# Kernel optimization log

Hardware: AMD Instinct MI355X
Metric: run time of the kernel (lower is better)

Reference implementation:

```python
import jax, jax.numpy as jnp
import numpy as np

EPS = 1e-3  # keras LayerNormalization default epsilon


def layer_norm(x, gamma, beta):
    mean = jnp.mean(x, axis=-1, keepdims=True)
    var = jnp.var(x, axis=-1, keepdims=True)
    return (x - mean) * jax.lax.rsqrt(var + EPS) * gamma + beta


def setup_inputs() -> dict:
    key = jax.random.key(0)
    ks = jax.random.split(key, 8)
    B, H, W, C = 16, 64, 64, 512
    IC = C // 8  # intermediate_channel = 64
    x = jax.random.normal(ks[0], (B, H, W, C), dtype=jnp.float32)
    s = 1.0 / np.sqrt(C)
    w_f = jax.random.normal(ks[1], (C, IC), dtype=jnp.float32) * s
    w_h = jax.random.normal(ks[2], (C, IC), dtype=jnp.float32) * s
    w_fgh = jax.random.normal(ks[3], (IC, C), dtype=jnp.float32) / np.sqrt(IC)
    gamma_f = jnp.ones((IC,), jnp.float32)
    beta_f = jnp.zeros((IC,), jnp.float32)
    gamma_h = jnp.ones((IC,), jnp.float32)
    beta_h = jnp.zeros((IC,), jnp.float32)
    gamma_fgh = jnp.ones((C,), jnp.float32)
    beta_fgh = jnp.zeros((C,), jnp.float32)
    scale = jnp.ones((1,), jnp.float32)  # non-negative scalar gate
    return {"x": x, "w_f": w_f, "w_h": w_h, "w_fgh": w_fgh,
            "gamma_f": gamma_f, "beta_f": beta_f,
            "gamma_h": gamma_h, "beta_h": beta_h,
            "gamma_fgh": gamma_fgh, "beta_fgh": beta_fgh,
            "scale": scale}


def reference(x, w_f, w_h, w_fgh, gamma_f, beta_f, gamma_h, beta_h,
              gamma_fgh, beta_fgh, scale):
    # NOTE: faithful to the source, which (re)uses w_f/LN_f for BOTH f and g,
    # and combines f and g with an ELEMENTWISE multiply (not a matmul).
    g = layer_norm(jnp.einsum("bhwc,ci->bhwi", x, w_f), gamma_f, beta_f)  # (B,H,W,IC)
    f = jnp.transpose(g, (0, 2, 1, 3))  # Permute(2,1,3): (B,W,H,IC)
    h = layer_norm(jnp.einsum("bhwc,ci->bhwi", x, w_h), gamma_h, beta_h)
    a = jax.nn.softmax(f * g, axis=1)  # softmax over axis 1 (H==W required)
    y = jnp.einsum("bhwi,ic->bhwc", a * h, w_fgh)
    y = layer_norm(y, gamma_fgh, beta_fgh) * scale  # scalar gate
    return x + y  # residual add
```

## Files before the change

### kernel.cpp

```cpp
#include <hip/hip_runtime.h>

#define EPSN 1e-3f

typedef __attribute__((ext_vector_type(8))) short short8;
typedef __attribute__((ext_vector_type(4))) float floatx4;

__device__ __forceinline__ unsigned f2bf_pack(float a, float b) {
    unsigned ua = __builtin_bit_cast(unsigned, a);
    ua += 0x7FFF + ((ua >> 16) & 1);
    unsigned ub = __builtin_bit_cast(unsigned, b);
    ub += 0x7FFF + ((ub >> 16) & 1);
    return (ua >> 16) | (ub & 0xFFFF0000u);
}
__device__ __forceinline__ unsigned short f2bf(float f) {
    unsigned u = __builtin_bit_cast(unsigned, f);
    u += 0x7FFF + ((u >> 16) & 1);
    return (unsigned short)(u >> 16);
}
__device__ __forceinline__ float bf2f(unsigned short u) {
    unsigned v = ((unsigned)u) << 16;
    return __builtin_bit_cast(float, v);
}

__global__ void k0_convert(const float* __restrict__ w_f,
                           const float* __restrict__ w_h,
                           const float* __restrict__ w_fgh,
                           unsigned short* __restrict__ Wgh,
                           unsigned short* __restrict__ Wf3)
{
    int tid = blockIdx.x * 256 + threadIdx.x;
    if (tid < 8192) {
        int n16 = tid & 15, k8 = (tid >> 4) & 63, ntile = tid >> 10;
        int n = ntile * 16 + n16;
        const float* src = (n < 64) ? (w_f + n) : (w_h + (n - 64));
        unsigned short o[8];
        #pragma unroll
        for (int j = 0; j < 8; ++j) o[j] = f2bf(src[(size_t)(k8 * 8 + j) * 64]);
        *(uint4*)&Wgh[(size_t)tid * 8] = *(const uint4*)o;
    } else if (tid < 12288) {
        int id = tid - 8192;
        int n16 = id & 15, k8 = (id >> 4) & 7, ntile = id >> 7;
        int n = ntile * 16 + n16;
        unsigned short o[8];
        #pragma unroll
        for (int j = 0; j < 8; ++j) o[j] = f2bf(w_fgh[(size_t)(k8 * 8 + j) * 512 + n]);
        *(uint4*)&Wf3[(size_t)id * 8] = *(const uint4*)o;
    }
}

__global__ __launch_bounds__(256, 4) void k1_gemm_ln(
    const float* __restrict__ x,
    const unsigned short* __restrict__ Wgh,
    const float* __restrict__ gamma_f, const float* __restrict__ beta_f,
    const float* __restrict__ gamma_h, const float* __restrict__ beta_h,
    float* __restrict__ g_out, unsigned short* __restrict__ h_out)
{
    const int t = threadIdx.x;
    const int lane = t & 63;
    const int wv = t >> 6;
    const int quad = lane >> 4;
    const int n16 = lane & 15;
    const int row_base = blockIdx.x * 64 + wv * 16;

    floatx4 acc[8];
    #pragma unroll
    for (int ct = 0; ct < 8; ++ct) acc[ct] = (floatx4){0.f, 0.f, 0.f, 0.f};

    const float* xrow = x + (size_t)(row_base + n16) * 512 + quad * 8;

    float4 u = *(const float4*)(xrow);
    float4 v = *(const float4*)(xrow + 4);

    #pragma unroll
    for (int c = 0; c < 16; ++c) {
        float4 un = u, vn = v;
        if (c < 15) {
            un = *(const float4*)(xrow + (c + 1) * 32);
            vn = *(const float4*)(xrow + (c + 1) * 32 + 4);
        }
        union { short8 s; uint4 q; } cvt;
        cvt.q = make_uint4(f2bf_pack(u.x, u.y), f2bf_pack(u.z, u.w),
                           f2bf_pack(v.x, v.y), f2bf_pack(v.z, v.w));
        short8 a = cvt.s;
        #pragma unroll
        for (int ct = 0; ct < 8; ++ct) {
            short8 b = *(const short8*)&Wgh[(size_t)(((ct * 64) + c * 4 + quad) * 16 + n16) * 8];
            acc[ct] = __builtin_amdgcn_mfma_f32_16x16x32_bf16(a, b, acc[ct], 0, 0, 0);
        }
        u = un; v = vn;
    }

    #pragma unroll
    for (int half = 0; half < 2; ++half) {
        float s[4] = {0.f, 0.f, 0.f, 0.f}, s2[4] = {0.f, 0.f, 0.f, 0.f};
        #pragma unroll
        for (int c0 = 0; c0 < 4; ++c0) {
            int ct = half * 4 + c0;
            #pragma unroll
            for (int r = 0; r < 4; ++r) {
                float val = acc[ct][r];
                s[r] += val; s2[r] += val * val;
            }
        }
        #pragma unroll
        for (int off = 1; off <= 8; off <<= 1)
            #pragma unroll
            for (int r = 0; r < 4; ++r) {
                s[r]  += __shfl_xor(s[r],  off, 64);
                s2[r] += __shfl_xor(s2[r], off, 64);
            }
        float mean[4], rstd[4];
        #pragma unroll
        for (int r = 0; r < 4; ++r) {
            mean[r] = s[r] * (1.f / 64.f);
            float var = s2[r] * (1.f / 64.f) - mean[r] * mean[r];
            rstd[r] = rsqrtf(var + EPSN);
        }
        #pragma unroll
        for (int c0 = 0; c0 < 4; ++c0) {
            int ct = half * 4 + c0;
            int col = c0 * 16 + n16;
            float gm = half ? gamma_h[col] : gamma_f[col];
            float bt = half ? beta_h[col]  : beta_f[col];
            #pragma unroll
            for (int r = 0; r < 4; ++r) {
                int row = row_base + quad * 4 + r;
                float val = (acc[ct][r] - mean[r]) * rstd[r] * gm + bt;
                if (half == 0)
                    g_out[(size_t)row * 64 + col] = val;
                else
                    h_out[(size_t)row * 64 + col] = f2bf(val);
            }
        }
    }
}

__global__ __launch_bounds__(256, 4) void k2_softmax(
    const float* __restrict__ g_in,
    const unsigned short* __restrict__ h_in,
    unsigned short* __restrict__ t_out)
{
    __shared__ float S[64 * 64];
    __shared__ float Hm[64 * 64];
    __shared__ float pmax[4 * 64];
    __shared__ float psum[4 * 64];
    __shared__ float colmax[64];
    __shared__ float colinv[64];

    const int t = threadIdx.x;
    const int b = blockIdx.x >> 6;
    const int w = blockIdx.x & 63;
    const size_t base1 = (size_t)(b * 64 + w) * 4096;

    #pragma unroll
    for (int i = 0; i < 16; ++i) {
        int e = t + i * 256;
        int hh = e >> 6, ii = e & 63;
        size_t idx2 = ((size_t)((b * 64 + hh) * 64 + w)) * 64 + ii;
        S[e]  = g_in[base1 + e] * g_in[idx2];
        Hm[e] = bf2f(h_in[idx2]);
    }
    __syncthreads();

    const int q = t >> 6;
    const int i = t & 63;
    float m = -1e30f;
    #pragma unroll
    for (int r = 0; r < 16; ++r)
        m = fmaxf(m, S[(q * 16 + r) * 64 + i]);
    pmax[q * 64 + i] = m;
    __syncthreads();
    if (t < 64)
        colmax[i] = fmaxf(fmaxf(pmax[i], pmax[64 + i]),
                          fmaxf(pmax[128 + i], pmax[192 + i]));
    __syncthreads();
    const float cm = colmax[i];
    float s = 0.f;
    #pragma unroll
    for (int r = 0; r < 16; ++r) {
        int idx = (q * 16 + r) * 64 + i;
        float e = __expf(S[idx] - cm);
        S[idx] = e;
        s += e;
    }
    psum[q * 64 + i] = s;
    __syncthreads();
    if (t < 64)
        colinv[i] = 1.f / (psum[i] + psum[64 + i] + psum[128 + i] + psum[192 + i]);
    __syncthreads();
    const float ci = colinv[i];
    #pragma unroll
    for (int r = 0; r < 16; ++r) {
        int hh = q * 16 + r;
        int idx = hh * 64 + i;
        size_t row_g = (size_t)((b * 64 + hh) * 64 + w);
        t_out[row_g * 64 + i] = f2bf(S[idx] * ci * Hm[idx]);
    }
}

__global__ __launch_bounds__(256, 4) void k3_gemm_ln_res(
    const unsigned short* __restrict__ tmat,
    const unsigned short* __restrict__ Wf3,
    const float* __restrict__ gamma, const float* __restrict__ beta,
    const float* __restrict__ scale,
    const float* __restrict__ x,
    float* __restrict__ out)
{
    __shared__ float bounce[4][16 * 132];
    __shared__ float2 exch[4][16];

    const int t = threadIdx.x;
    const int lane = t & 63;
    const int wv = t >> 6;
    const int quad = lane >> 4;
    const int n16 = lane & 15;
    const int rowtile = blockIdx.x * 2 + (wv >> 1);
    const int half = wv & 1;

    const unsigned short* trow = tmat + (size_t)(rowtile * 16 + n16) * 64 + quad * 8;
    short8 a0 = *(const short8*)trow;
    short8 a1 = *(const short8*)(trow + 32);

    floatx4 acc[16];
    #pragma unroll
    for (int nt = 0; nt < 16; ++nt) acc[nt] = (floatx4){0.f, 0.f, 0.f, 0.f};
    #pragma unroll
    for (int nt = 0; nt < 16; ++nt) {
        int ngt = half * 16 + nt;
        short8 b0 = *(const short8*)&Wf3[(size_t)((ngt * 8 + quad) * 16 + n16) * 8];
        short8 b1 = *(const short8*)&Wf3[(size_t)((ngt * 8 + 4 + quad) * 16 + n16) * 8];
        acc[nt] = __builtin_amdgcn_mfma_f32_16x16x32_bf16(a0, b0, acc[nt], 0, 0, 0);
        acc[nt] = __builtin_amdgcn_mfma_f32_16x16x32_bf16(a1, b1, acc[nt], 0, 0, 0);
    }

    float s[4] = {0.f, 0.f, 0.f, 0.f}, s2[4] = {0.f, 0.f, 0.f, 0.f};
    #pragma unroll
    for (int nt = 0; nt < 16; ++nt)
        #pragma unroll
        for (int r = 0; r < 4; ++r) {
            float v = acc[nt][r];
            s[r] += v; s2[r] += v * v;
        }
    #pragma unroll
    for (int off = 1; off <= 8; off <<= 1)
        #pragma unroll
        for (int r = 0; r < 4; ++r) {
            s[r]  += __shfl_xor(s[r],  off, 64);
            s2[r] += __shfl_xor(s2[r], off, 64);
        }
    if (n16 == 0) {
        #pragma unroll
        for (int r = 0; r < 4; ++r)
            exch[wv][quad * 4 + r] = make_float2(s[r], s2[r]);
    }
    __syncthreads();
    float mean[4], rstd[4];
    #pragma unroll
    for (int r = 0; r < 4; ++r) {
        float2 o = exch[wv ^ 1][quad * 4 + r];
        float st = s[r] + o.x, st2 = s2[r] + o.y;
        mean[r] = st * (1.f / 512.f);
        float var = st2 * (1.f / 512.f) - mean[r] * mean[r];
        rstd[r] = rsqrtf(var + EPSN);
    }
    const float sc = scale[0];

    #pragma unroll
    for (int chunk = 0; chunk < 2; ++chunk) {
        __syncthreads();
        #pragma unroll
        for (int n0 = 0; n0 < 8; ++n0) {
            int nt = chunk * 8 + n0;
            int col = half * 256 + nt * 16 + n16;
            float gm = gamma[col], bt = beta[col];
            #pragma unroll
            for (int r = 0; r < 4; ++r)
                bounce[wv][(quad * 4 + r) * 132 + n0 * 16 + n16] =
                    sc * ((acc[nt][r] - mean[r]) * rstd[r] * gm + bt);
        }
        __syncthreads();
        #pragma unroll
        for (int pass = 0; pass < 8; ++pass) {
            int row = pass * 2 + (lane >> 5);
            int coff = (lane & 31) * 4;
            float4 v = *(const float4*)&bounce[wv][row * 132 + coff];
            size_t gidx = ((size_t)rowtile * 16 + row) * 512 + half * 256 + chunk * 128 + coff;
            float4 xv = *(const float4*)&x[gidx];
            float4 o;
            o.x = xv.x + v.x; o.y = xv.y + v.y; o.z = xv.z + v.z; o.w = xv.w + v.w;
            *(float4*)&out[gidx] = o;
        }
    }
}

extern "C" void kernel_launch(void* const* d_in, const int* in_sizes, int n_in,
                              void* d_out, int out_size, void* d_ws, size_t ws_size,
                              hipStream_t stream) {
    const float* x         = (const float*)d_in[0];
    const float* w_f       = (const float*)d_in[1];
    const float* w_h       = (const float*)d_in[2];
    const float* w_fgh     = (const float*)d_in[3];
    const float* gamma_f   = (const float*)d_in[4];
    const float* beta_f    = (const float*)d_in[5];
    const float* gamma_h   = (const float*)d_in[6];
    const float* beta_h    = (const float*)d_in[7];
    const float* gamma_fgh = (const float*)d_in[8];
    const float* beta_fgh  = (const float*)d_in[9];
    const float* scale     = (const float*)d_in[10];
    float* out = (float*)d_out;

    char* wsb = (char*)d_ws;
    float* g            = (float*)wsb;
    unsigned short* h   = (unsigned short*)(wsb + 16777216);
    unsigned short* tm  = (unsigned short*)(wsb + 25165824);
    unsigned short* Wgh = (unsigned short*)(wsb + 33554432);
    unsigned short* Wf3 = (unsigned short*)(wsb + 33685504);

    k0_convert<<<48, 256, 0, stream>>>(w_f, w_h, w_fgh, Wgh, Wf3);
    k1_gemm_ln<<<1024, 256, 0, stream>>>(x, Wgh, gamma_f, beta_f,
                                         gamma_h, beta_h, g, h);
    k2_softmax<<<1024, 256, 0, stream>>>(g, h, tm);
    k3_gemm_ln_res<<<2048, 256, 0, stream>>>(tm, Wf3, gamma_fgh, beta_fgh,
                                             scale, x, out);
}
```

Baseline: 310.6 us.

## Stage Wgh B-tiles through double-buffered LDS via global_load_lds in k1

```diff
diff --git a/kernel.cpp b/kernel.cpp
--- a/kernel.cpp
+++ b/kernel.cpp
@@ -20,6 +20,13 @@
 __device__ __forceinline__ float bf2f(unsigned short u) {
     unsigned v = ((unsigned)u) << 16;
     return __builtin_bit_cast(float, v);
+}
+
+__device__ __forceinline__ void gload_lds16(const unsigned short* g, unsigned short* l) {
+    __builtin_amdgcn_global_load_lds(
+        (const __attribute__((address_space(1))) unsigned int*)g,
+        (__attribute__((address_space(3))) unsigned int*)l,
+        16, 0, 0);
 }
 
 __global__ void k0_convert(const float* __restrict__ w_f,
@@ -55,6 +62,8 @@
     const float* __restrict__ gamma_h, const float* __restrict__ beta_h,
     float* __restrict__ g_out, unsigned short* __restrict__ h_out)
 {
+    __shared__ unsigned short Blds[2][8192];
+
     const int t = threadIdx.x;
     const int lane = t & 63;
     const int wv = t >> 6;
@@ -67,27 +76,53 @@
     for (int ct = 0; ct < 8; ++ct) acc[ct] = (floatx4){0.f, 0.f, 0.f, 0.f};
 
     const float* xrow = x + (size_t)(row_base + n16) * 512 + quad * 8;
-
-    float4 u = *(const float4*)(xrow);
-    float4 v = *(const float4*)(xrow + 4);
-
-    #pragma unroll
-    for (int c = 0; c < 16; ++c) {
-        float4 un = u, vn = v;
-        if (c < 15) {
-            un = *(const float4*)(xrow + (c + 1) * 32);
-            vn = *(const float4*)(xrow + (c + 1) * 32 + 4);
-        }
-        union { short8 s; uint4 q; } cvt;
-        cvt.q = make_uint4(f2bf_pack(u.x, u.y), f2bf_pack(u.z, u.w),
-                           f2bf_pack(v.x, v.y), f2bf_pack(v.z, v.w));
-        short8 a = cvt.s;
-        #pragma unroll
-        for (int ct = 0; ct < 8; ++ct) {
-            short8 b = *(const short8*)&Wgh[(size_t)(((ct * 64) + c * 4 + quad) * 16 + n16) * 8];
-            acc[ct] = __builtin_amdgcn_mfma_f32_16x16x32_bf16(a, b, acc[ct], 0, 0, 0);
-        }
-        u = un; v = vn;
+    const unsigned short* bsrc = Wgh + (size_t)lane * 8;
+
+    auto stage = [&](int par, int ch) {
+        #pragma unroll
+        for (int i = 0; i < 4; ++i) {
+            int s = wv * 4 + i;
+            int cl = s >> 3, ct = s & 7;
+            gload_lds16(bsrc + (size_t)ct * 8192 + (ch * 2 + cl) * 512,
+                        &Blds[par][s * 512]);
+        }
+    };
+
+    stage(0, 0);
+    float4 u[2], v[2];
+    u[0] = *(const float4*)(xrow);
+    v[0] = *(const float4*)(xrow + 4);
+    u[1] = *(const float4*)(xrow + 32);
+    v[1] = *(const float4*)(xrow + 36);
+    __syncthreads();
+
+    #pragma unroll
+    for (int ch = 0; ch < 8; ++ch) {
+        const int par = ch & 1;
+        if (ch < 7) stage(par ^ 1, ch + 1);
+        float4 un[2], vn[2];
+        if (ch < 7) {
+            un[0] = *(const float4*)(xrow + ch * 64 + 64);
+            vn[0] = *(const float4*)(xrow + ch * 64 + 68);
+            un[1] = *(const float4*)(xrow + ch * 64 + 96);
+            vn[1] = *(const float4*)(xrow + ch * 64 + 100);
+        }
+        #pragma unroll
+        for (int cl = 0; cl < 2; ++cl) {
+            union { short8 s; uint4 q; } cvt;
+            cvt.q = make_uint4(f2bf_pack(u[cl].x, u[cl].y), f2bf_pack(u[cl].z, u[cl].w),
+                               f2bf_pack(v[cl].x, v[cl].y), f2bf_pack(v[cl].z, v[cl].w));
+            short8 a = cvt.s;
+            #pragma unroll
+            for (int ct = 0; ct < 8; ++ct) {
+                short8 b = *(const short8*)&Blds[par][(cl * 8 + ct) * 512 + lane * 8];
+                acc[ct] = __builtin_amdgcn_mfma_f32_16x16x32_bf16(a, b, acc[ct], 0, 0, 0);
+            }
+        }
+        if (ch < 7) {
+            u[0] = un[0]; v[0] = vn[0]; u[1] = un[1]; v[1] = vn[1];
+        }
+        __syncthreads();
     }
 
     #pragma unroll
```

After: 297.2 us. 4.3% less time.
